# Performance work log

Hardware: AMD Instinct MI355X
Metric: run time of the kernel (lower is better)

The kernel has to match this reference:

```python
import jax, jax.numpy as jnp
import numpy as np

B, TAU, T0V, D, PD, RD, DO, K = 2048, 32, 96, 64, 3, 1, 64, 16
R = 1.0  # radius for radius_graph


def setup_inputs() -> dict:
    key = jax.random.key(0)
    ks = jax.random.split(key, 9)
    return {
        "x": jax.random.normal(ks[0], (B, TAU, D), jnp.float32),
        "pos": jax.random.uniform(ks[1], (B, TAU, PD), jnp.float32),
        "rot": jax.random.uniform(ks[2], (B, TAU, RD), jnp.float32),
        "old_x": jax.random.normal(ks[3], (B, 128, D), jnp.float32),
        "old_pos": jax.random.uniform(ks[4], (B, 128, PD), jnp.float32),
        "old_rot": jax.random.uniform(ks[5], (B, 128, RD), jnp.float32),
        "W_self": jax.random.normal(ks[6], (D + PD + RD, DO), jnp.float32) * 0.1,
        "W_nbr": jax.random.normal(ks[7], (D + PD + RD, DO), jnp.float32) * 0.1,
        "bias": jax.random.normal(ks[8], (DO,), jnp.float32) * 0.1,
        "T0": T0V,
        "tau": TAU,
    }


def reference(x, pos, rot, old_x, old_pos, old_rot, W_self, W_nbr, bias, T0, tau):
    # --- update(): scatter new observations into the state buffers ---
    # (regular case: T[b]=T0, taus[b]=tau for all b, so new_idx is a static slice)
    new_x = old_x.at[:, T0:T0 + tau].set(x)
    new_pos = old_pos.at[:, T0:T0 + tau].set(pos)
    new_rot = old_rot.at[:, T0:T0 + tau].set(rot)

    L = T0 + tau  # valid (non-padded) nodes per env
    nx, npv, nr = new_x[:, :L], new_pos[:, :L], new_rot[:, :L]
    h = jnp.concatenate([nx, npv, nr], axis=-1)  # [B, L, D+PD+RD] node features

    # --- radius_graph(r, max_num_neighbors=K, loop=True) + remove_noncausal_edges ---
    # edge (j -> i) kept iff ||pos_j - pos_i|| <= r and j < i (causal, drops self-loops)
    diff = npv[:, :, None, :] - npv[:, None, :, :]           # [B, L, L, PD]
    d2 = jnp.sum(diff * diff, axis=-1)                        # [B, L, L] (target i, source j)
    t_idx = jnp.arange(L)
    causal = t_idx[None, :] < t_idx[:, None]                  # [L, L] j < i
    mask = causal[None, :, :] & (d2 <= R * R)
    masked_d2 = jnp.where(mask, d2, jnp.inf)
    neg_d, nbr_idx = jax.lax.top_k(-masked_d2, K)             # k nearest causal in-radius
    valid = jnp.isfinite(neg_d)                               # [B, L, K]

    # --- gnn(): one message-passing layer (stand-in for external gnn) ---
    msg = h @ W_nbr                                           # [B, L, DO]
    gathered = jax.vmap(lambda m, i: m[i])(msg, nbr_idx)      # [B, L, K, DO]
    agg = jnp.sum(gathered * valid[..., None].astype(msg.dtype), axis=2)
    out = jax.nn.relu(h @ W_self + agg + bias)                # [B, L, DO]

    # --- gather flat_new_idx / scatter into padded output ---
    padded_output = out[:, T0:T0 + tau]                       # [B, tau, DO]
    return padded_output, new_x, new_pos, new_rot
```

## Files before the change

### kernel.cpp

```cpp
#include <hip/hip_runtime.h>
#include <hip/hip_bf16.h>
#include <cstdint>
#include <cstddef>

#define NB 2048
#define TAU 32
#define T0C 96
#define LQ 128
#define DD 64
#define DOUT 64
#define KK 16
#define INVK 0xFFFFFFFFu

typedef unsigned long long u64;
typedef unsigned int u32;
typedef __attribute__((ext_vector_type(8))) short short8;
typedef __attribute__((ext_vector_type(4))) float f32x4;

__device__ __forceinline__ float fmul_exact(float a, float b) {
  float r; asm("v_mul_f32 %0, %1, %2" : "=v"(r) : "v"(a), "v"(b)); return r;
}
__device__ __forceinline__ float fadd_exact(float a, float b) {
  float r; asm("v_add_f32 %0, %1, %2" : "=v"(r) : "v"(a), "v"(b)); return r;
}
__device__ __forceinline__ unsigned short f2bf(float f) {
  __hip_bfloat16 h = __float2bfloat16(f);
  return *reinterpret_cast<unsigned short*>(&h);
}
__device__ __forceinline__ u32 shfl_xor_u32(u32 v, int mask) {
  return (u32)__shfl_xor((int)v, mask, 64);
}

__device__ __forceinline__ void barrier_lgkm() {
  asm volatile("s_waitcnt lgkmcnt(0)" ::: "memory");
  __builtin_amdgcn_s_barrier();
  __builtin_amdgcn_sched_barrier(0);
}

#define CA(i, j) { u32 _lo = min(kd[i], kd[j]); u32 _hi = max(kd[i], kd[j]); kd[i] = _lo; kd[j] = _hi; }
#define CD(i, j) { u32 _lo = min(kd[i], kd[j]); u32 _hi = max(kd[i], kd[j]); kd[i] = _hi; kd[j] = _lo; }

#define SORT16() do { \
  CA(0,1)  CD(2,3)  CA(4,5)  CD(6,7)  CA(8,9)  CD(10,11) CA(12,13) CD(14,15) \
  CA(0,2)  CA(1,3)  CD(4,6)  CD(5,7)  CA(8,10) CA(9,11)  CD(12,14) CD(13,15) \
  CA(0,1)  CA(2,3)  CD(4,5)  CD(6,7)  CA(8,9)  CA(10,11) CD(12,13) CD(14,15) \
  CA(0,4)  CA(1,5)  CA(2,6)  CA(3,7)  CD(8,12) CD(9,13)  CD(10,14) CD(11,15) \
  CA(0,2)  CA(1,3)  CA(4,6)  CA(5,7)  CD(8,10) CD(9,11)  CD(12,14) CD(13,15) \
  CA(0,1)  CA(2,3)  CA(4,5)  CA(6,7)  CD(8,9)  CD(10,11) CD(12,13) CD(14,15) \
  CA(0,8)  CA(1,9)  CA(2,10) CA(3,11) CA(4,12) CA(5,13)  CA(6,14)  CA(7,15)  \
  CA(0,4)  CA(1,5)  CA(2,6)  CA(3,7)  CA(8,12) CA(9,13)  CA(10,14) CA(11,15) \
  CA(0,2)  CA(1,3)  CA(4,6)  CA(5,7)  CA(8,10) CA(9,11)  CA(12,14) CA(13,15) \
  CA(0,1)  CA(2,3)  CA(4,5)  CA(6,7)  CA(8,9)  CA(10,11) CA(12,13) CA(14,15) \
} while (0)

#define MERGE16() do { \
  CA(0,8)  CA(1,9)  CA(2,10) CA(3,11) CA(4,12) CA(5,13)  CA(6,14)  CA(7,15)  \
  CA(0,4)  CA(1,5)  CA(2,6)  CA(3,7)  CA(8,12) CA(9,13)  CA(10,14) CA(11,15) \
  CA(0,2)  CA(1,3)  CA(4,6)  CA(5,7)  CA(8,10) CA(9,11)  CA(12,14) CA(13,15) \
  CA(0,1)  CA(2,3)  CA(4,5)  CA(6,7)  CA(8,9)  CA(10,11) CA(12,13) CA(14,15) \
} while (0)

#define SHUF_MERGE(mask) do { \
  u32 pb[16]; \
  _Pragma("unroll") \
  for (int _i = 0; _i < 16; ++_i) pb[_i] = shfl_xor_u32(kd[15 - _i], mask); \
  _Pragma("unroll") \
  for (int _i = 0; _i < 16; ++_i) kd[_i] = min(kd[_i], pb[_i]); \
  MERGE16(); \
} while (0)

__global__ __launch_bounds__(256) void prep_w(
    const float* __restrict__ W_nbr, const float* __restrict__ W_self,
    unsigned short* __restrict__ wst) {
  int idx = blockIdx.x * 256 + threadIdx.x;
  int m = idx & 4095;
  int n = m >> 6, k = m & 63;
  const float* src = (idx < 4096) ? W_nbr : W_self;
  wst[idx] = f2bf(src[k * DOUT + n]);
}

__global__ __launch_bounds__(256, 4) void navgcm_fused(
    const float* __restrict__ x, const float* __restrict__ pos_in, const float* __restrict__ rot_in,
    const float* __restrict__ old_x, const float* __restrict__ old_pos, const float* __restrict__ old_rot,
    const float* __restrict__ W_self, const float* __restrict__ W_nbr, const float* __restrict__ bias,
    const unsigned short* __restrict__ wst,
    float* __restrict__ outp)
{
  const int b = blockIdx.x;
  const int tid = threadIdx.x;
  const int lane = tid & 63;
  const int wv = tid >> 6;
  const int fr = lane & 15;
  const int fg = lane >> 4;

  __shared__ __align__(16) unsigned char uni[33792];
  __shared__ float px[LQ], py[LQ], pz[LQ], rt[LQ];
  __shared__ uint4 selidx[32];

  unsigned short (*Hs)[72] = reinterpret_cast<unsigned short(*)[72]>(uni);
  float (*msgs)[66] = reinterpret_cast<float(*)[66]>(uni);

  const bool haspos = tid < LQ;
  float p0 = 0.f, p1 = 0.f, p2 = 0.f, rr = 0.f;
  if (haspos) {
    int t = tid;
    if (t < T0C) {
      const float* s = old_pos + ((size_t)b * LQ + t) * 3;
      p0 = s[0]; p1 = s[1]; p2 = s[2];
      rr = old_rot[(size_t)b * LQ + t];
    } else {
      const float* s = pos_in + ((size_t)b * TAU + (t - T0C)) * 3;
      p0 = s[0]; p1 = s[1]; p2 = s[2];
      rr = rot_in[(size_t)b * TAU + (t - T0C)];
    }
  }

  float4 v[8];
  #pragma unroll
  for (int it = 0; it < 8; ++it) {
    int n = tid + 256 * it;
    int row = n >> 4, c4 = n & 15;
    const float4* src = (row < T0C)
        ? (const float4*)(old_x + ((size_t)b * LQ + row) * DD)
        : (const float4*)(x + ((size_t)b * TAU + (row - T0C)) * DD);
    v[it] = src[c4];
  }

  float* dpos = outp + (size_t)NB * TAU * DOUT + (size_t)NB * LQ * DD;
  float* drot = dpos + (size_t)NB * LQ * 3;
  if (haspos) {
    px[tid] = p0; py[tid] = p1; pz[tid] = p2; rt[tid] = rr;
    size_t g = (size_t)b * LQ + tid;
    dpos[g * 3 + 0] = p0; dpos[g * 3 + 1] = p1; dpos[g * 3 + 2] = p2;
    drot[g] = rr;
  }
  barrier_lgkm();

  {
    const int q = tid >> 3, s8 = tid & 7;
    const int i = T0C + q;
    const float pix = px[i], piy = py[i], piz = pz[i];

    u32 kb[16];
    #pragma unroll
    for (int c = 0; c < 16; ++c) {
      int j = 8 * c + s8;
      float dx = pix - px[j], dy = piy - py[j], dz = piz - pz[j];
      float d2 = fadd_exact(fadd_exact(fmul_exact(dx, dx), fmul_exact(dy, dy)),
                            fmul_exact(dz, dz));
      bool valid = (d2 <= 1.0f) && (j < i);
      kb[c] = valid ? __float_as_uint(d2) : INVK;
    }

    u32 kd[16];
    #pragma unroll
    for (int c = 0; c < 16; ++c) kd[c] = kb[c];
    SORT16();
    SHUF_MERGE(1);
    SHUF_MERGE(2);
    SHUF_MERGE(4);

    const u32 T = kd[15];
    int nless = 0;
    #pragma unroll
    for (int t = 0; t < KK; ++t) nless += (kd[t] < T) ? 1 : 0;
    const int needT = (T == INVK) ? 0 : (KK - nless);

    u32 selmask = 0;
    #pragma unroll
    for (int c = 0; c < 16; ++c) selmask |= (kb[c] < T) ? (1u << c) : 0u;

    u32 em = 0;
    #pragma unroll
    for (int c = 0; c < 16; ++c) em |= (kb[c] == T) ? (1u << c) : 0u;
    if (T == INVK) em = 0;
    for (int t = 0; __any(t < needT); ++t) {
      bool act = t < needT;
      u32 myj = (act && em) ? (u32)(8 * __builtin_ctz(em) + s8) : 0xFFFFu;
      u32 gj = myj;
      gj = min(gj, shfl_xor_u32(gj, 1));
      gj = min(gj, shfl_xor_u32(gj, 2));
      gj = min(gj, shfl_xor_u32(gj, 4));
      if (act && myj == gj && myj != 0xFFFFu) {
        int c = __builtin_ctz(em);
        selmask |= 1u << c;
        em &= em - 1;
      }
    }

    if (s8 < 4) ((u32*)selidx)[q * 4 + s8] = 0x7F7F7F7Fu;
    int cnt = __builtin_popcount(selmask);
    int pre = 0;
    #pragma unroll
    for (int k = 0; k < 7; ++k) {
      int vt = __shfl(cnt, (lane & ~7) + k, 64);
      pre += (k < s8) ? vt : 0;
    }
    unsigned char* sp = (unsigned char*)selidx + q * 16 + pre;
    u32 m = selmask;
    while (m) {
      int c = __builtin_ctz(m);
      m &= m - 1;
      *sp++ = (unsigned char)(8 * c + s8);
    }
  }

  float4* dnx = (float4*)(outp + (size_t)NB * TAU * DOUT);
  #pragma unroll
  for (int it = 0; it < 8; ++it) {
    int n = tid + 256 * it;
    int row = n >> 4, c4 = n & 15;
    ushort4 w4;
    w4.x = f2bf(v[it].x); w4.y = f2bf(v[it].y); w4.z = f2bf(v[it].z); w4.w = f2bf(v[it].w);
    *reinterpret_cast<ushort4*>(&Hs[row][c4 * 4]) = w4;
    dnx[(size_t)b * 2048 + n] = v[it];
  }
  barrier_lgkm();

  const unsigned short* wn_t = wst;
  const unsigned short* ws_t = wst + 4096;

  short8 bW[4][2];
  #pragma unroll
  for (int nt = 0; nt < 4; ++nt)
    #pragma unroll
    for (int ks = 0; ks < 2; ++ks)
      bW[nt][ks] = *reinterpret_cast<const short8*>(&wn_t[(nt * 16 + fr) * 64 + ks * 32 + fg * 8]);

  f32x4 acc[2][4];
  #pragma unroll
  for (int m = 0; m < 2; ++m)
    #pragma unroll
    for (int n = 0; n < 4; ++n)
      acc[m][n] = (f32x4){0.f, 0.f, 0.f, 0.f};

  #pragma unroll
  for (int mtl = 0; mtl < 2; ++mtl) {
    int mrow = (2 * wv + mtl) * 16;
    short8 a0 = *reinterpret_cast<const short8*>(&Hs[mrow + fr][fg * 8]);
    short8 a1 = *reinterpret_cast<const short8*>(&Hs[mrow + fr][32 + fg * 8]);
    #pragma unroll
    for (int nt = 0; nt < 4; ++nt) {
      acc[mtl][nt] = __builtin_amdgcn_mfma_f32_16x16x32_bf16(a0, bW[nt][0], acc[mtl][nt], 0, 0, 0);
      acc[mtl][nt] = __builtin_amdgcn_mfma_f32_16x16x32_bf16(a1, bW[nt][1], acc[mtl][nt], 0, 0, 0);
    }
  }

  const int mt = wv & 1;
  const int ntb = (wv >> 1) * 2;
  short8 aQ0 = *reinterpret_cast<const short8*>(&Hs[T0C + mt * 16 + fr][fg * 8]);
  short8 aQ1 = *reinterpret_cast<const short8*>(&Hs[T0C + mt * 16 + fr][32 + fg * 8]);
  f32x4 acc2[2];
  #pragma unroll
  for (int n = 0; n < 2; ++n) acc2[n] = (f32x4){0.f, 0.f, 0.f, 0.f};
  #pragma unroll
  for (int ntl = 0; ntl < 2; ++ntl) {
    int nt = ntb + ntl;
    short8 b0 = *reinterpret_cast<const short8*>(&ws_t[(nt * 16 + fr) * 64 + fg * 8]);
    short8 b1 = *reinterpret_cast<const short8*>(&ws_t[(nt * 16 + fr) * 64 + 32 + fg * 8]);
    acc2[ntl] = __builtin_amdgcn_mfma_f32_16x16x32_bf16(aQ0, b0, acc2[ntl], 0, 0, 0);
    acc2[ntl] = __builtin_amdgcn_mfma_f32_16x16x32_bf16(aQ1, b1, acc2[ntl], 0, 0, 0);
  }
  barrier_lgkm();

  float wn4[4][4];
  #pragma unroll
  for (int nt = 0; nt < 4; ++nt) {
    int col = nt * 16 + fr;
    wn4[nt][0] = W_nbr[64 * DOUT + col];
    wn4[nt][1] = W_nbr[65 * DOUT + col];
    wn4[nt][2] = W_nbr[66 * DOUT + col];
    wn4[nt][3] = W_nbr[67 * DOUT + col];
  }
  #pragma unroll
  for (int mtl = 0; mtl < 2; ++mtl) {
    #pragma unroll
    for (int r = 0; r < 4; ++r) {
      int row = (2 * wv + mtl) * 16 + fg * 4 + r;
      float q0 = px[row], q1 = py[row], q2 = pz[row], q3 = rt[row];
      #pragma unroll
      for (int nt = 0; nt < 4; ++nt) {
        float vv = acc[mtl][nt][r]
                 + q0 * wn4[nt][0] + q1 * wn4[nt][1] + q2 * wn4[nt][2] + q3 * wn4[nt][3];
        msgs[row][nt * 16 + fr] = (row == LQ - 1) ? 0.f : vv;
      }
    }
  }
  barrier_lgkm();

  #pragma unroll
  for (int ntl = 0; ntl < 2; ++ntl) {
    int col = (ntb + ntl) * 16 + fr;
    float ws0 = W_self[64 * DOUT + col], ws1 = W_self[65 * DOUT + col];
    float ws2 = W_self[66 * DOUT + col], ws3 = W_self[67 * DOUT + col];
    float bi = bias[col];
    #pragma unroll
    for (int r = 0; r < 4; ++r) {
      int q = mt * 16 + fg * 4 + r;
      int row = T0C + q;
      uint4 sv = selidx[q];
      float agg = 0.f;
      #pragma unroll
      for (int s = 0; s < KK; ++s) {
        u32 wd = (s < 4) ? sv.x : (s < 8) ? sv.y : (s < 12) ? sv.z : sv.w;
        int j = (wd >> ((s & 3) * 8)) & 0xff;
        agg += msgs[j][col];
      }
      float vv = acc2[ntl][r] + agg + bi
               + px[row] * ws0 + py[row] * ws1 + pz[row] * ws2 + rt[row] * ws3;
      vv = fmaxf(vv, 0.f);
      outp[((size_t)b * TAU + q) * DOUT + col] = vv;
    }
  }
}

extern "C" void kernel_launch(void* const* d_in, const int* in_sizes, int n_in,
                              void* d_out, int out_size, void* d_ws, size_t ws_size,
                              hipStream_t stream) {
  (void)in_sizes; (void)n_in; (void)ws_size; (void)out_size;
  const float* x       = (const float*)d_in[0];
  const float* pos     = (const float*)d_in[1];
  const float* rot     = (const float*)d_in[2];
  const float* old_x   = (const float*)d_in[3];
  const float* old_pos = (const float*)d_in[4];
  const float* old_rot = (const float*)d_in[5];
  const float* W_self  = (const float*)d_in[6];
  const float* W_nbr   = (const float*)d_in[7];
  const float* bias    = (const float*)d_in[8];
  float* out = (float*)d_out;
  unsigned short* wst = (unsigned short*)d_ws;

  hipLaunchKernelGGL(prep_w, dim3(32), dim3(256), 0, stream, W_nbr, W_self, wst);
  hipLaunchKernelGGL(navgcm_fused, dim3(NB), dim3(256), 0, stream,
                     x, pos, rot, old_x, old_pos, old_rot, W_self, W_nbr, bias, wst, out);
}
```

Measured before the change: 44.45 us.

## Replace neighbor gather-sum with MFMA against a one-hot selection matrix

Turns the selected-neighbor aggregation into a dense bf16 MFMA. A 32x128 one-hot selection matrix in shared memory is multiplied by a transposed bf16 message matrix, replacing the per-output 16-way indexed LDS gather and the prefix-sum index compaction. Messages are stored in bf16 instead of fp32, which shrinks LDS use and lets launch bounds target 5 blocks per CU. This adds bf16 rounding of messages, which may change numerical accuracy, and it adds the cost of zero-filling the selection matrix.

```diff
diff --git a/kernel.cpp b/kernel.cpp
--- a/kernel.cpp
+++ b/kernel.cpp
@@ -79,7 +79,7 @@
   wst[idx] = f2bf(src[k * DOUT + n]);
 }
 
-__global__ __launch_bounds__(256, 4) void navgcm_fused(
+__global__ __launch_bounds__(256, 5) void navgcm_fused(
     const float* __restrict__ x, const float* __restrict__ pos_in, const float* __restrict__ rot_in,
     const float* __restrict__ old_x, const float* __restrict__ old_pos, const float* __restrict__ old_rot,
     const float* __restrict__ W_self, const float* __restrict__ W_nbr, const float* __restrict__ bias,
@@ -93,12 +93,12 @@
   const int fr = lane & 15;
   const int fg = lane >> 4;
 
-  __shared__ __align__(16) unsigned char uni[33792];
+  __shared__ __align__(16) unsigned char uni[18432];
+  __shared__ __align__(16) unsigned short Pm[32][136];
   __shared__ float px[LQ], py[LQ], pz[LQ], rt[LQ];
-  __shared__ uint4 selidx[32];
 
   unsigned short (*Hs)[72] = reinterpret_cast<unsigned short(*)[72]>(uni);
-  float (*msgs)[66] = reinterpret_cast<float(*)[66]>(uni);
+  unsigned short (*msgsT)[136] = reinterpret_cast<unsigned short(*)[136]>(uni);
 
   const bool haspos = tid < LQ;
   float p0 = 0.f, p1 = 0.f, p2 = 0.f, rr = 0.f;
@@ -124,6 +124,15 @@
         ? (const float4*)(old_x + ((size_t)b * LQ + row) * DD)
         : (const float4*)(x + ((size_t)b * TAU + (row - T0C)) * DD);
     v[it] = src[c4];
+  }
+
+  {
+    u32* pz32 = (u32*)&Pm[0][0];
+    #pragma unroll
+    for (int k = 0; k < 9; ++k) {
+      int idx = tid + 256 * k;
+      if (idx < 2176) pz32[idx] = 0u;
+    }
   }
 
   float* dpos = outp + (size_t)NB * TAU * DOUT + (size_t)NB * LQ * DD;
@@ -188,20 +197,11 @@
       }
     }
 
-    if (s8 < 4) ((u32*)selidx)[q * 4 + s8] = 0x7F7F7F7Fu;
-    int cnt = __builtin_popcount(selmask);
-    int pre = 0;
-    #pragma unroll
-    for (int k = 0; k < 7; ++k) {
-      int vt = __shfl(cnt, (lane & ~7) + k, 64);
-      pre += (k < s8) ? vt : 0;
-    }
-    unsigned char* sp = (unsigned char*)selidx + q * 16 + pre;
     u32 m = selmask;
     while (m) {
       int c = __builtin_ctz(m);
       m &= m - 1;
-      *sp++ = (unsigned char)(8 * c + s8);
+      Pm[q][8 * c + s8] = 0x3F80;
     }
   }
 
@@ -261,6 +261,11 @@
     acc2[ntl] = __builtin_amdgcn_mfma_f32_16x16x32_bf16(aQ0, b0, acc2[ntl], 0, 0, 0);
     acc2[ntl] = __builtin_amdgcn_mfma_f32_16x16x32_bf16(aQ1, b1, acc2[ntl], 0, 0, 0);
   }
+
+  short8 pa[4];
+  #pragma unroll
+  for (int ks = 0; ks < 4; ++ks)
+    pa[ks] = *reinterpret_cast<const short8*>(&Pm[mt * 16 + fr][ks * 32 + fg * 8]);
   barrier_lgkm();
 
   float wn4[4][4];
@@ -274,19 +279,43 @@
   }
   #pragma unroll
   for (int mtl = 0; mtl < 2; ++mtl) {
+    int rowb = (2 * wv + mtl) * 16 + fg * 4;
+    float q0[4], q1[4], q2[4], q3[4];
     #pragma unroll
     for (int r = 0; r < 4; ++r) {
-      int row = (2 * wv + mtl) * 16 + fg * 4 + r;
-      float q0 = px[row], q1 = py[row], q2 = pz[row], q3 = rt[row];
+      q0[r] = px[rowb + r]; q1[r] = py[rowb + r];
+      q2[r] = pz[rowb + r]; q3[r] = rt[rowb + r];
+    }
+    #pragma unroll
+    for (int nt = 0; nt < 4; ++nt) {
+      int col = nt * 16 + fr;
+      ushort4 w4;
+      unsigned short* wp = (unsigned short*)&w4;
       #pragma unroll
-      for (int nt = 0; nt < 4; ++nt) {
+      for (int r = 0; r < 4; ++r) {
         float vv = acc[mtl][nt][r]
-                 + q0 * wn4[nt][0] + q1 * wn4[nt][1] + q2 * wn4[nt][2] + q3 * wn4[nt][3];
-        msgs[row][nt * 16 + fr] = (row == LQ - 1) ? 0.f : vv;
+                 + q0[r] * wn4[nt][0] + q1[r] * wn4[nt][1]
+                 + q2[r] * wn4[nt][2] + q3[r] * wn4[nt][3];
+        wp[r] = f2bf(vv);
       }
+      if (rowb + 3 == LQ - 1) wp[3] = 0;
+      *reinterpret_cast<ushort4*>(&msgsT[col][rowb]) = w4;
     }
   }
   barrier_lgkm();
+
+  f32x4 agg4[2];
+  #pragma unroll
+  for (int n = 0; n < 2; ++n) agg4[n] = (f32x4){0.f, 0.f, 0.f, 0.f};
+  #pragma unroll
+  for (int ntl = 0; ntl < 2; ++ntl) {
+    int col16 = (ntb + ntl) * 16 + fr;
+    #pragma unroll
+    for (int ks = 0; ks < 4; ++ks) {
+      short8 pb = *reinterpret_cast<const short8*>(&msgsT[col16][ks * 32 + fg * 8]);
+      agg4[ntl] = __builtin_amdgcn_mfma_f32_16x16x32_bf16(pa[ks], pb, agg4[ntl], 0, 0, 0);
+    }
+  }
 
   #pragma unroll
   for (int ntl = 0; ntl < 2; ++ntl) {
@@ -298,15 +327,7 @@
     for (int r = 0; r < 4; ++r) {
       int q = mt * 16 + fg * 4 + r;
       int row = T0C + q;
-      uint4 sv = selidx[q];
-      float agg = 0.f;
-      #pragma unroll
-      for (int s = 0; s < KK; ++s) {
-        u32 wd = (s < 4) ? sv.x : (s < 8) ? sv.y : (s < 12) ? sv.z : sv.w;
-        int j = (wd >> ((s & 3) * 8)) & 0xff;
-        agg += msgs[j][col];
-      }
-      float vv = acc2[ntl][r] + agg + bi
+      float vv = acc2[ntl][r] + agg4[ntl][r] + bi
                + px[row] * ws0 + py[row] * ws1 + pz[row] * ws2 + rt[row] * ws3;
       vv = fmaxf(vv, 0.f);
       outp[((size_t)b * TAU + q) * DOUT + col] = vv;
```

Result: slower. 54.32 us (+22.2%).
